# Kernel optimization log

Measured on AMD Instinct MI355X. Metric: run time of the kernel, lower is better.

The kernel has to match this reference:

```python
import jax, jax.numpy as jnp
import numpy as np
from functools import partial

H = 51

def lstm_cell(x, h, c, W_ih, W_hh, b_ih, b_hh):
    # PyTorch LSTMCell: gates ordered (i, f, g, o)
    z = x @ W_ih.T + b_ih + h @ W_hh.T + b_hh  # [B, 4H]
    i, f, g, o = jnp.split(z, 4, axis=-1)
    i = jax.nn.sigmoid(i)
    f = jax.nn.sigmoid(f)
    g = jnp.tanh(g)
    o = jax.nn.sigmoid(o)
    c_new = f * c + i * g
    h_new = o * jnp.tanh(c_new)
    return h_new, c_new


def setup_inputs() -> dict:
    key = jax.random.key(0)
    ks = jax.random.split(key, 12)
    B, T = 2048, 512
    s = 1.0 / np.sqrt(H)  # PyTorch default init scale
    inp = {
        "input": jax.random.normal(ks[0], (B, T), dtype=jnp.float32),
        "W_ih1": jax.random.uniform(ks[1], (4 * H, 1), jnp.float32, -s, s),
        "W_hh1": jax.random.uniform(ks[2], (4 * H, H), jnp.float32, -s, s),
        "b_ih1": jax.random.uniform(ks[3], (4 * H,), jnp.float32, -s, s),
        "b_hh1": jax.random.uniform(ks[4], (4 * H,), jnp.float32, -s, s),
        "W_ih2": jax.random.uniform(ks[5], (4 * H, H), jnp.float32, -s, s),
        "W_hh2": jax.random.uniform(ks[6], (4 * H, H), jnp.float32, -s, s),
        "b_ih2": jax.random.uniform(ks[7], (4 * H,), jnp.float32, -s, s),
        "b_hh2": jax.random.uniform(ks[8], (4 * H,), jnp.float32, -s, s),
        "W_lin": jax.random.uniform(ks[9], (1, H), jnp.float32, -s, s),
        "b_lin": jax.random.uniform(ks[10], (1,), jnp.float32, -s, s),
        "future": 32,
    }
    return inp


def reference(input, W_ih1, W_hh1, b_ih1, b_hh1, W_ih2, W_hh2, b_ih2, b_hh2, W_lin, b_lin, future):
    B, T = input.shape
    dt = input.dtype
    h1 = jnp.zeros((B, H), dt)
    c1 = jnp.zeros((B, H), dt)
    h2 = jnp.zeros((B, H), dt)
    c2 = jnp.zeros((B, H), dt)

    def core(carry, x_t):
        h1, c1, h2, c2 = carry
        h1, c1 = lstm_cell(x_t, h1, c1, W_ih1, W_hh1, b_ih1, b_hh1)
        h2, c2 = lstm_cell(h1, h2, c2, W_ih2, W_hh2, b_ih2, b_hh2)
        out = h2 @ W_lin.T + b_lin  # [B, 1]
        return (h1, c1, h2, c2), out

    xs = input.T[:, :, None]  # [T, B, 1]
    carry, outs = jax.lax.scan(core, (h1, c1, h2, c2), xs)

    def fstep(carry, _):
        state, out = carry
        new_state, new_out = core(state, out)
        return (new_state, new_out), new_out

    last_out = outs[-1]
    _, fouts = jax.lax.scan(fstep, (carry, last_out), None, length=future)

    all_outs = jnp.concatenate([outs, fouts], axis=0)  # [T+future, B, 1]
    return all_outs[:, :, 0].T  # [B, T+future]
```

## Files before the change

kernel.cpp:

```cpp
#include <hip/hip_runtime.h>

#define H 51
#define TIN 512
#define TTOT 544
#define BTILE 8
#define AST 88
#define H2ST 13
#define SOST 548
#define NTHR 768

typedef __attribute__((ext_vector_type(8))) short short8;
typedef __attribute__((ext_vector_type(4))) float float4v;

#define MFMA __builtin_amdgcn_mfma_f32_16x16x32_bf16

__device__ __forceinline__ float fast_rcp(float x) { return __builtin_amdgcn_rcpf(x); }
__device__ __forceinline__ float sigf(float x)  { return fast_rcp(1.0f + __expf(-x)); }
__device__ __forceinline__ float tanhf_(float x){ return 1.0f - 2.0f * fast_rcp(1.0f + __expf(2.0f * x)); }

__device__ __forceinline__ unsigned short bf16rnd(float x) {
    unsigned int u = __float_as_uint(x);
    return (unsigned short)((u + 0x7fffu + ((u >> 16) & 1u)) >> 16);
}
__device__ __forceinline__ unsigned int bf16pk(float a, float b) {
    unsigned int r;
    asm("v_cvt_pk_bf16_f32 %0, %1, %2" : "=v"(r) : "v"(a), "v"(b));
    return r;
}
__device__ __forceinline__ void bf16split(float x, unsigned short& hi, float& lo) {
    unsigned int u  = __float_as_uint(x);
    unsigned int hr = (u + 0x7fffu + ((u >> 16) & 1u)) & 0xffff0000u;
    hi = (unsigned short)(hr >> 16);
    lo = x - __uint_as_float(hr);
}

__device__ __forceinline__ float b1val(int k, int u, int g,
                                       const float* Whh1, const float* Wih1) {
    if (u >= H) return 0.0f;
    const int r = g * H + u;
    if (k < H)  return Whh1[r * H + k];
    if (k == H) return Wih1[r];
    return 0.0f;
}
__device__ __forceinline__ float b2val(int k, int u, int g,
                                       const float* Wih2, const float* Whh2) {
    if (u >= H) return 0.0f;
    const int r = g * H + u;
    if (k < H) return Wih2[r * H + k];
    if (k >= 64 && k < 64 + H) return Whh2[r * H + (k - 64)];
    return 0.0f;
}

__global__ __launch_bounds__(NTHR)
__attribute__((amdgpu_waves_per_eu(3, 3)))
void lstm_seq(
    const float* __restrict__ input,
    const float* __restrict__ W_ih1,
    const float* __restrict__ W_hh1,
    const float* __restrict__ b_ih1,
    const float* __restrict__ b_hh1,
    const float* __restrict__ W_ih2,
    const float* __restrict__ W_hh2,
    const float* __restrict__ b_ih2,
    const float* __restrict__ b_hh2,
    const float* __restrict__ W_lin,
    const float* __restrict__ b_lin,
    float* __restrict__ out)
{
    __shared__ __align__(16) unsigned short sA1h[2][16][AST];
    __shared__ __align__(16) unsigned short sA2h[2][16][AST];
    __shared__ float sH2f[2][64][H2ST];
    __shared__ __align__(8) float sXlo[2][8];
    __shared__ float sWlin[64];
    __shared__ __align__(16) float sIn[BTILE][TIN];
    __shared__ __align__(16) float sOut[BTILE][SOST];

    const int tid  = threadIdx.x;
    const int lane = tid & 63;
    const int wv   = tid >> 6;
    const int ut   = wv & 3;
    const int quad = lane >> 4;
    const int kq   = quad * 8;
    const int nl   = lane & 15;
    const int u    = ut * 16 + nl;
    const int ur   = (u < H) ? u : (H - 1);
    const int b0   = blockIdx.x * BTILE;
    const float blin = b_lin[0];
    const int rowA = (quad & 1) * 4 + (quad >> 1) * 2;
    const int arow = quad * 4;
    const int kc   = lane & 31;
    const int bhead= 2 * ut + (lane >> 5);

    {
        unsigned short* p0 = &sA1h[0][0][0];
        unsigned short* p2 = &sA2h[0][0][0];
        for (int i = tid; i < 2 * 16 * AST; i += NTHR) { p0[i] = 0; p2[i] = 0; }
        float* pf = &sH2f[0][0][0];
        for (int i = tid; i < 2 * 64 * H2ST; i += NTHR) pf[i] = 0.0f;
        if (tid < 16) sXlo[tid >> 3][tid & 7] = 0.0f;
        if (tid < 64) sWlin[tid] = (tid < H) ? W_lin[tid] : 0.0f;
        for (int i = tid; i < BTILE * (TIN / 4); i += NTHR) {
            const int r = i >> 7, c = i & 127;
            *(float4v*)&sIn[r][c * 4] =
                *(const float4v*)&input[(size_t)(b0 + r) * TIN + c * 4];
        }
    }
    __syncthreads();
    if (tid < 8) {
        unsigned short hh; float lo;
        bf16split(sIn[tid][0], hh, lo);
        sA1h[0][(tid & 2) ? tid + 6 : tid][51] = hh;
        sXlo[0][tid] = lo;
    }
    __syncthreads();

    if (wv < 4) {
        short8 B1h[4][2];
        float zb1[4], wxf[4];
        #pragma unroll
        for (int g = 0; g < 4; ++g) {
            #pragma unroll
            for (int kt = 0; kt < 2; ++kt)
                #pragma unroll
                for (int j = 0; j < 8; ++j)
                    B1h[g][kt][j] = (short)bf16rnd(b1val(kt * 32 + kq + j, u, g, W_hh1, W_ih1));
            const int r = g * H + ur;
            zb1[g] = b_ih1[r] + b_hh1[r];
            wxf[g] = W_ih1[r];
        }
        float c1[2] = {0, 0};

        auto l1work = [&](int rs, int ws) __attribute__((always_inline)) {
            short8 a0h = *(const short8*)&sA1h[rs][nl][kq];
            short8 a1h = *(const short8*)&sA1h[rs][nl][32 + kq];
            float2 xl = *(const float2*)&sXlo[rs][rowA];
            float4v C[4];
            #pragma unroll
            for (int g = 0; g < 4; ++g) {
                float4v c = {zb1[g], zb1[g], zb1[g], zb1[g]};
                c = MFMA(a0h, B1h[g][0], c, 0, 0, 0);
                c = MFMA(a1h, B1h[g][1], c, 0, 0, 0);
                C[g] = c;
            }
            float h1v[2];
            #pragma unroll
            for (int j = 0; j < 2; ++j) {
                const float xr = j ? xl.y : xl.x;
                float I = sigf  (C[0][j] + wxf[0] * xr);
                float F = sigf  (C[1][j] + wxf[1] * xr);
                float G = tanhf_(C[2][j] + wxf[2] * xr);
                float O = sigf  (C[3][j] + wxf[3] * xr);
                c1[j] = F * c1[j] + I * G;
                h1v[j] = O * tanhf_(c1[j]);
            }
            if (u < H) {
                const unsigned int pk = bf16pk(h1v[0], h1v[1]);
                sA1h[ws][arow][u]     = (unsigned short)pk;
                sA1h[ws][arow + 1][u] = (unsigned short)(pk >> 16);
            }
        };

        for (int s = 0; s < TIN; ++s) {
            if ((s & 1) == 0) l1work(0, 1);
            else              l1work(1, 0);
            __syncthreads();
        }
        for (int s = TIN; s <= TTOT; ++s) {
            const int rs = s & 1, ws = rs ^ 1;
            __syncthreads();
            __syncthreads();
            if (s < TTOT) l1work(rs, ws);
            __syncthreads();
        }
    } else if (wv < 8) {
        short8 B2h[4][4];
        float zb2[4];
        #pragma unroll
        for (int g = 0; g < 4; ++g) {
            #pragma unroll
            for (int kt = 0; kt < 4; ++kt)
                #pragma unroll
                for (int j = 0; j < 8; ++j)
                    B2h[g][kt][j] = (short)bf16rnd(b2val(kt * 32 + kq + j, u, g, W_ih2, W_hh2));
            const int r = g * H + ur;
            zb2[g] = b_ih2[r] + b_hh2[r];
        }
        float c2[2] = {0, 0};

        auto l2work = [&](int rs, int ws) __attribute__((always_inline)) {
            short8 f0h = *(const short8*)&sA1h[rs][nl][kq];
            short8 f1h = *(const short8*)&sA1h[rs][nl][32 + kq];
            short8 f2h = *(const short8*)&sA2h[rs][nl][kq];
            short8 f3h = *(const short8*)&sA2h[rs][nl][32 + kq];
            float4v C[4];
            #pragma unroll
            for (int g = 0; g < 4; ++g) {
                float4v c = {zb2[g], zb2[g], zb2[g], zb2[g]};
                c = MFMA(f0h, B2h[g][0], c, 0, 0, 0);
                c = MFMA(f1h, B2h[g][1], c, 0, 0, 0);
                c = MFMA(f2h, B2h[g][2], c, 0, 0, 0);
                c = MFMA(f3h, B2h[g][3], c, 0, 0, 0);
                C[g] = c;
            }
            float h2v[2];
            #pragma unroll
            for (int j = 0; j < 2; ++j) {
                float I = sigf  (C[0][j]);
                float F = sigf  (C[1][j]);
                float G = tanhf_(C[2][j]);
                float O = sigf  (C[3][j]);
                c2[j] = F * c2[j] + I * G;
                h2v[j] = O * tanhf_(c2[j]);
            }
            if (u < H) {
                const unsigned int pk = bf16pk(h2v[0], h2v[1]);
                sA2h[ws][arow][u]     = (unsigned short)pk;
                sA2h[ws][arow + 1][u] = (unsigned short)(pk >> 16);
                sH2f[rs][u][rowA]     = h2v[0];
                sH2f[rs][u][rowA + 1] = h2v[1];
            }
        };

        for (int s = 0; s < TIN; ++s) {
            if ((s & 1) == 0) { if (s) l2work(0, 1); }
            else              l2work(1, 0);
            __syncthreads();
        }
        for (int s = TIN; s <= TTOT; ++s) {
            const int rs = s & 1, ws = rs ^ 1;
            l2work(rs, ws);
            __syncthreads();
            __syncthreads();
            __syncthreads();
        }
    } else {
        auto headw = [&](int slot, int outt) __attribute__((always_inline)) -> float {
            float p = sWlin[kc]      * sH2f[slot][kc][bhead]
                    + sWlin[kc + 32] * sH2f[slot][kc + 32][bhead];
            p += __shfl_xor(p, 1);  p += __shfl_xor(p, 2);  p += __shfl_xor(p, 4);
            p += __shfl_xor(p, 8);  p += __shfl_xor(p, 16);
            float val = p + blin;
            if (kc == 0) sOut[bhead][outt] = val;
            return val;
        };

        for (int s = 0; s < TIN; ++s) {
            const int ws = (s & 1) ? 0 : 1;
            if (s >= 2) headw(ws, s - 2);
            if ((wv == 8) && (lane < 8) && (s + 1 < TIN)) {
                unsigned short hh; float lo; bf16split(sIn[lane][s + 1], hh, lo);
                sA1h[ws][(lane & 2) ? lane + 6 : lane][51] = hh;
                sXlo[ws][lane] = lo;
            }
            __syncthreads();
        }
        for (int s = TIN; s <= TTOT; ++s) {
            const int rs = s & 1, ws = rs ^ 1;
            __syncthreads();
            {
                float val = headw(rs, s - 1);
                if (kc == 0 && s < TTOT) {
                    unsigned short hh; float lo; bf16split(val, hh, lo);
                    sA1h[rs][(bhead & 2) ? bhead + 6 : bhead][51] = hh;
                    sXlo[rs][bhead] = lo;
                }
                if (s == TIN) headw(ws, s - 2);
            }
            __syncthreads();
            __syncthreads();
        }
    }

    __syncthreads();
    for (int i = tid; i < BTILE * (TTOT / 4); i += NTHR) {
        const int r = i / (TTOT / 4);
        const int c = i - r * (TTOT / 4);
        *(float4v*)&out[(size_t)(b0 + r) * TTOT + c * 4] =
            *(const float4v*)&sOut[r][c * 4];
    }
}

extern "C" void kernel_launch(void* const* d_in, const int* in_sizes, int n_in,
                              void* d_out, int out_size, void* d_ws, size_t ws_size,
                              hipStream_t stream) {
    const float* input = (const float*)d_in[0];
    const float* W_ih1 = (const float*)d_in[1];
    const float* W_hh1 = (const float*)d_in[2];
    const float* b_ih1 = (const float*)d_in[3];
    const float* b_hh1 = (const float*)d_in[4];
    const float* W_ih2 = (const float*)d_in[5];
    const float* W_hh2 = (const float*)d_in[6];
    const float* b_ih2 = (const float*)d_in[7];
    const float* b_hh2 = (const float*)d_in[8];
    const float* W_lin = (const float*)d_in[9];
    const float* b_lin = (const float*)d_in[10];
    float* out = (float*)d_out;

    lstm_seq<<<dim3(256), dim3(NTHR), 0, stream>>>(input, W_ih1, W_hh1, b_ih1, b_hh1,
                                                   W_ih2, W_hh2, b_ih2, b_hh2,
                                                   W_lin, b_lin, out);
}
```

Before: 390.3 us.

## Replace block barriers with LDS counter spin-waits and triple buffering in teacher-forced phase

In the 512-step input phase, the per-step __syncthreads between the layer-1, layer-2 and head warp groups are replaced by shared-memory counters. Each group bumps its counter after a step and spin-waits (with s_sleep) on the counters it depends on. The state buffers go from double to triple slots, so producers can run one step ahead of consumers without overwriting data still being read. This aims to decouple the groups and hide barrier stalls, at the cost of polling overhead and subtle memory-ordering risk, since it relies on lgkmcnt waits and volatile reads.

After: 469.8 us. +20.4%, slower.

```diff
diff --git a/kernel.cpp b/kernel.cpp
--- a/kernel.cpp
+++ b/kernel.cpp
@@ -8,6 +8,7 @@
 #define H2ST 13
 #define SOST 548
 #define NTHR 768
+#define NSLOT 3
 
 typedef __attribute__((ext_vector_type(8))) short short8;
 typedef __attribute__((ext_vector_type(4))) float float4v;
@@ -67,13 +68,14 @@
     const float* __restrict__ b_lin,
     float* __restrict__ out)
 {
-    __shared__ __align__(16) unsigned short sA1h[2][16][AST];
-    __shared__ __align__(16) unsigned short sA2h[2][16][AST];
-    __shared__ float sH2f[2][64][H2ST];
-    __shared__ __align__(8) float sXlo[2][8];
+    __shared__ __align__(16) unsigned short sA1h[NSLOT][16][AST];
+    __shared__ __align__(16) unsigned short sA2h[NSLOT][16][AST];
+    __shared__ float sH2f[NSLOT][64][H2ST];
+    __shared__ __align__(8) float sXlo[NSLOT][8];
     __shared__ float sWlin[64];
     __shared__ __align__(16) float sIn[BTILE][TIN];
     __shared__ __align__(16) float sOut[BTILE][SOST];
+    __shared__ int sCnt[4];
 
     const int tid  = threadIdx.x;
     const int lane = tid & 63;
@@ -91,14 +93,25 @@
     const int kc   = lane & 31;
     const int bhead= 2 * ut + (lane >> 5);
 
+    volatile int* vc = (volatile int*)sCnt;
+    auto spin = [&](int idx, int v) __attribute__((always_inline)) {
+        while (vc[idx] < v) __builtin_amdgcn_s_sleep(1);
+        asm volatile("" ::: "memory");
+    };
+    auto bump = [&](int idx) __attribute__((always_inline)) {
+        asm volatile("s_waitcnt lgkmcnt(0)" ::: "memory");
+        if (lane == 0) atomicAdd(&sCnt[idx], 1);
+    };
+
     {
         unsigned short* p0 = &sA1h[0][0][0];
         unsigned short* p2 = &sA2h[0][0][0];
-        for (int i = tid; i < 2 * 16 * AST; i += NTHR) { p0[i] = 0; p2[i] = 0; }
+        for (int i = tid; i < NSLOT * 16 * AST; i += NTHR) { p0[i] = 0; p2[i] = 0; }
         float* pf = &sH2f[0][0][0];
-        for (int i = tid; i < 2 * 64 * H2ST; i += NTHR) pf[i] = 0.0f;
-        if (tid < 16) sXlo[tid >> 3][tid & 7] = 0.0f;
+        for (int i = tid; i < NSLOT * 64 * H2ST; i += NTHR) pf[i] = 0.0f;
+        if (tid < NSLOT * 8) sXlo[tid >> 3][tid & 7] = 0.0f;
         if (tid < 64) sWlin[tid] = (tid < H) ? W_lin[tid] : 0.0f;
+        if (tid == 0) { sCnt[0] = 0; sCnt[1] = 4; sCnt[2] = 0; }
         for (int i = tid; i < BTILE * (TIN / 4); i += NTHR) {
             const int r = i >> 7, c = i & 127;
             *(float4v*)&sIn[r][c * 4] =
@@ -160,13 +173,19 @@
             }
         };
 
-        for (int s = 0; s < TIN; ++s) {
-            if ((s & 1) == 0) l1work(0, 1);
-            else              l1work(1, 0);
-            __syncthreads();
-        }
+        {
+            int si = 0, so = 1, t1 = 0;
+            for (int s = 0; s < TIN; ++s) {
+                spin(0, t1); spin(2, t1); spin(1, t1 - 4);
+                l1work(si, so);
+                bump(0);
+                t1 += 4;
+                si = so; so = (so == 2) ? 0 : so + 1;
+            }
+        }
+        __syncthreads();
         for (int s = TIN; s <= TTOT; ++s) {
-            const int rs = s & 1, ws = rs ^ 1;
+            const int rs = s % 3, ws = (s + 1) % 3;
             __syncthreads();
             __syncthreads();
             if (s < TTOT) l1work(rs, ws);
@@ -221,13 +240,19 @@
             }
         };
 
-        for (int s = 0; s < TIN; ++s) {
-            if ((s & 1) == 0) { if (s) l2work(0, 1); }
-            else              l2work(1, 0);
-            __syncthreads();
-        }
+        {
+            int si = 1, so = 2, t4 = 4;
+            for (int t = 1; t < TIN; ++t) {
+                spin(0, t4); spin(1, t4); spin(2, t4 - 4);
+                l2work(si, so);
+                bump(1);
+                t4 += 4;
+                si = so; so = (so == 2) ? 0 : so + 1;
+            }
+        }
+        __syncthreads();
         for (int s = TIN; s <= TTOT; ++s) {
-            const int rs = s & 1, ws = rs ^ 1;
+            const int rs = s % 3, ws = (s + 1) % 3;
             l2work(rs, ws);
             __syncthreads();
             __syncthreads();
@@ -244,18 +269,25 @@
             return val;
         };
 
-        for (int s = 0; s < TIN; ++s) {
-            const int ws = (s & 1) ? 0 : 1;
-            if (s >= 2) headw(ws, s - 2);
-            if ((wv == 8) && (lane < 8) && (s + 1 < TIN)) {
-                unsigned short hh; float lo; bf16split(sIn[lane][s + 1], hh, lo);
-                sA1h[ws][(lane & 2) ? lane + 6 : lane][51] = hh;
-                sXlo[ws][lane] = lo;
-            }
-            __syncthreads();
-        }
+        {
+            int sm1 = 2, so = 1, t4 = 0;
+            for (int s = 0; s < TIN; ++s) {
+                spin(0, t4 - 4);
+                if (s >= 2) { spin(1, t4); headw(sm1, s - 2); }
+                if ((wv == 8) && (lane < 8) && (s + 1 < TIN)) {
+                    unsigned short hh; float lo; bf16split(sIn[lane][s + 1], hh, lo);
+                    sA1h[so][(lane & 2) ? lane + 6 : lane][51] = hh;
+                    sXlo[so][lane] = lo;
+                }
+                bump(2);
+                t4 += 4;
+                sm1 = (sm1 == 2) ? 0 : sm1 + 1;
+                so  = (so  == 2) ? 0 : so + 1;
+            }
+        }
+        __syncthreads();
         for (int s = TIN; s <= TTOT; ++s) {
-            const int rs = s & 1, ws = rs ^ 1;
+            const int rs = s % 3;
             __syncthreads();
             {
                 float val = headw(rs, s - 1);
@@ -264,7 +296,7 @@
                     sA1h[rs][(bhead & 2) ? bhead + 6 : bhead][51] = hh;
                     sXlo[rs][bhead] = lo;
                 }
-                if (s == TIN) headw(ws, s - 2);
+                if (s == TIN) headw((TIN - 1) % 3, s - 2);
             }
             __syncthreads();
             __syncthreads();
```

## Split LSTM gate nonlinearities across duplicated wave groups and merge head into layer-1 waves

Applied to the files above, without the earlier changes.

Raises the block to 16 waves: each layer now runs on two 4-wave groups that issue the same MFMAs, and each group handles only one of the two accumulator rows, which halves the per-thread transcendental work on the critical path. The separate head/input-feed waves are removed. The second layer-1 group now also computes the linear head and stages the next input. This trades redundant MFMA work and more waves per block for a shorter serial elementwise tail per timestep. The sIn row is padded so the input load becomes a single pass per thread.

Result: slower. 535.8 us (+37.3%).

```diff
diff --git a/kernel.cpp b/kernel.cpp
--- a/kernel.cpp
+++ b/kernel.cpp
@@ -6,8 +6,9 @@
 #define BTILE 8
 #define AST 88
 #define H2ST 13
+#define INST 516
 #define SOST 548
-#define NTHR 768
+#define NTHR 1024
 
 typedef __attribute__((ext_vector_type(8))) short short8;
 typedef __attribute__((ext_vector_type(4))) float float4v;
@@ -21,11 +22,6 @@
 __device__ __forceinline__ unsigned short bf16rnd(float x) {
     unsigned int u = __float_as_uint(x);
     return (unsigned short)((u + 0x7fffu + ((u >> 16) & 1u)) >> 16);
-}
-__device__ __forceinline__ unsigned int bf16pk(float a, float b) {
-    unsigned int r;
-    asm("v_cvt_pk_bf16_f32 %0, %1, %2" : "=v"(r) : "v"(a), "v"(b));
-    return r;
 }
 __device__ __forceinline__ void bf16split(float x, unsigned short& hi, float& lo) {
     unsigned int u  = __float_as_uint(x);
@@ -52,7 +48,7 @@
 }
 
 __global__ __launch_bounds__(NTHR)
-__attribute__((amdgpu_waves_per_eu(3, 3)))
+__attribute__((amdgpu_waves_per_eu(4, 4)))
 void lstm_seq(
     const float* __restrict__ input,
     const float* __restrict__ W_ih1,
@@ -72,13 +68,15 @@
     __shared__ float sH2f[2][64][H2ST];
     __shared__ __align__(8) float sXlo[2][8];
     __shared__ float sWlin[64];
-    __shared__ __align__(16) float sIn[BTILE][TIN];
+    __shared__ __align__(16) float sIn[BTILE][INST];
     __shared__ __align__(16) float sOut[BTILE][SOST];
 
     const int tid  = threadIdx.x;
     const int lane = tid & 63;
     const int wv   = tid >> 6;
+    const int grp  = wv >> 2;
     const int ut   = wv & 3;
+    const int jj   = grp & 1;
     const int quad = lane >> 4;
     const int kq   = quad * 8;
     const int nl   = lane & 15;
@@ -86,8 +84,8 @@
     const int ur   = (u < H) ? u : (H - 1);
     const int b0   = blockIdx.x * BTILE;
     const float blin = b_lin[0];
-    const int rowA = (quad & 1) * 4 + (quad >> 1) * 2;
-    const int arow = quad * 4;
+    const int rowAj = (quad & 1) * 4 + (quad >> 1) * 2 + jj;
+    const int arowj = quad * 4 + jj;
     const int kc   = lane & 31;
     const int bhead= 2 * ut + (lane >> 5);
 
@@ -99,8 +97,8 @@
         for (int i = tid; i < 2 * 64 * H2ST; i += NTHR) pf[i] = 0.0f;
         if (tid < 16) sXlo[tid >> 3][tid & 7] = 0.0f;
         if (tid < 64) sWlin[tid] = (tid < H) ? W_lin[tid] : 0.0f;
-        for (int i = tid; i < BTILE * (TIN / 4); i += NTHR) {
-            const int r = i >> 7, c = i & 127;
+        {
+            const int r = tid >> 7, c = tid & 127;
             *(float4v*)&sIn[r][c * 4] =
                 *(const float4v*)&input[(size_t)(b0 + r) * TIN + c * 4];
         }
@@ -114,7 +112,7 @@
     }
     __syncthreads();
 
-    if (wv < 4) {
+    if (grp < 2) {
         short8 B1h[4][2];
         float zb1[4], wxf[4];
         #pragma unroll
@@ -128,12 +126,12 @@
             zb1[g] = b_ih1[r] + b_hh1[r];
             wxf[g] = W_ih1[r];
         }
-        float c1[2] = {0, 0};
+        float c1 = 0.0f;
 
         auto l1work = [&](int rs, int ws) __attribute__((always_inline)) {
             short8 a0h = *(const short8*)&sA1h[rs][nl][kq];
             short8 a1h = *(const short8*)&sA1h[rs][nl][32 + kq];
-            float2 xl = *(const float2*)&sXlo[rs][rowA];
+            float xr = sXlo[rs][rowAj];
             float4v C[4];
             #pragma unroll
             for (int g = 0; g < 4; ++g) {
@@ -142,98 +140,14 @@
                 c = MFMA(a1h, B1h[g][1], c, 0, 0, 0);
                 C[g] = c;
             }
-            float h1v[2];
-            #pragma unroll
-            for (int j = 0; j < 2; ++j) {
-                const float xr = j ? xl.y : xl.x;
-                float I = sigf  (C[0][j] + wxf[0] * xr);
-                float F = sigf  (C[1][j] + wxf[1] * xr);
-                float G = tanhf_(C[2][j] + wxf[2] * xr);
-                float O = sigf  (C[3][j] + wxf[3] * xr);
-                c1[j] = F * c1[j] + I * G;
-                h1v[j] = O * tanhf_(c1[j]);
-            }
-            if (u < H) {
-                const unsigned int pk = bf16pk(h1v[0], h1v[1]);
-                sA1h[ws][arow][u]     = (unsigned short)pk;
-                sA1h[ws][arow + 1][u] = (unsigned short)(pk >> 16);
-            }
+            float I = sigf  (C[0][jj] + wxf[0] * xr);
+            float F = sigf  (C[1][jj] + wxf[1] * xr);
+            float G = tanhf_(C[2][jj] + wxf[2] * xr);
+            float O = sigf  (C[3][jj] + wxf[3] * xr);
+            c1 = F * c1 + I * G;
+            float h1v = O * tanhf_(c1);
+            if (u < H) sA1h[ws][arowj][u] = bf16rnd(h1v);
         };
-
-        for (int s = 0; s < TIN; ++s) {
-            if ((s & 1) == 0) l1work(0, 1);
-            else              l1work(1, 0);
-            __syncthreads();
-        }
-        for (int s = TIN; s <= TTOT; ++s) {
-            const int rs = s & 1, ws = rs ^ 1;
-            __syncthreads();
-            __syncthreads();
-            if (s < TTOT) l1work(rs, ws);
-            __syncthreads();
-        }
-    } else if (wv < 8) {
-        short8 B2h[4][4];
-        float zb2[4];
-        #pragma unroll
-        for (int g = 0; g < 4; ++g) {
-            #pragma unroll
-            for (int kt = 0; kt < 4; ++kt)
-                #pragma unroll
-                for (int j = 0; j < 8; ++j)
-                    B2h[g][kt][j] = (short)bf16rnd(b2val(kt * 32 + kq + j, u, g, W_ih2, W_hh2));
-            const int r = g * H + ur;
-            zb2[g] = b_ih2[r] + b_hh2[r];
-        }
-        float c2[2] = {0, 0};
-
-        auto l2work = [&](int rs, int ws) __attribute__((always_inline)) {
-            short8 f0h = *(const short8*)&sA1h[rs][nl][kq];
-            short8 f1h = *(const short8*)&sA1h[rs][nl][32 + kq];
-            short8 f2h = *(const short8*)&sA2h[rs][nl][kq];
-            short8 f3h = *(const short8*)&sA2h[rs][nl][32 + kq];
-            float4v C[4];
-            #pragma unroll
-            for (int g = 0; g < 4; ++g) {
-                float4v c = {zb2[g], zb2[g], zb2[g], zb2[g]};
-                c = MFMA(f0h, B2h[g][0], c, 0, 0, 0);
-                c = MFMA(f1h, B2h[g][1], c, 0, 0, 0);
-                c = MFMA(f2h, B2h[g][2], c, 0, 0, 0);
-                c = MFMA(f3h, B2h[g][3], c, 0, 0, 0);
-                C[g] = c;
-            }
-            float h2v[2];
-            #pragma unroll
-            for (int j = 0; j < 2; ++j) {
-                float I = sigf  (C[0][j]);
-                float F = sigf  (C[1][j]);
-                float G = tanhf_(C[2][j]);
-                float O = sigf  (C[3][j]);
-                c2[j] = F * c2[j] + I * G;
-                h2v[j] = O * tanhf_(c2[j]);
-            }
-            if (u < H) {
-                const unsigned int pk = bf16pk(h2v[0], h2v[1]);
-                sA2h[ws][arow][u]     = (unsigned short)pk;
-                sA2h[ws][arow + 1][u] = (unsigned short)(pk >> 16);
-                sH2f[rs][u][rowA]     = h2v[0];
-                sH2f[rs][u][rowA + 1] = h2v[1];
-            }
-        };
-
-        for (int s = 0; s < TIN; ++s) {
-            if ((s & 1) == 0) { if (s) l2work(0, 1); }
-            else              l2work(1, 0);
-            __syncthreads();
-        }
-        for (int s = TIN; s <= TTOT; ++s) {
-            const int rs = s & 1, ws = rs ^ 1;
-            l2work(rs, ws);
-            __syncthreads();
-            __syncthreads();
-            __syncthreads();
-        }
-    } else {
         auto headw = [&](int slot, int outt) __attribute__((always_inline)) -> float {
             float p = sWlin[kc]      * sH2f[slot][kc][bhead]
                     + sWlin[kc + 32] * sH2f[slot][kc + 32][bhead];
@@ -244,20 +158,32 @@
             return val;
         };
 
-        for (int s = 0; s < TIN; ++s) {
-            const int ws = (s & 1) ? 0 : 1;
-            if (s >= 2) headw(ws, s - 2);
-            if ((wv == 8) && (lane < 8) && (s + 1 < TIN)) {
-                unsigned short hh; float lo; bf16split(sIn[lane][s + 1], hh, lo);
-                sA1h[ws][(lane & 2) ? lane + 6 : lane][51] = hh;
-                sXlo[ws][lane] = lo;
-            }
-            __syncthreads();
+        if (grp == 0) {
+            for (int s = 0; s < TIN; ++s) {
+                if ((s & 1) == 0) l1work(0, 1);
+                else              l1work(1, 0);
+                __syncthreads();
+            }
+        } else {
+            for (int s = 0; s < TIN; ++s) {
+                const int rs = s & 1, ws = rs ^ 1;
+                float xpre = 0.0f;
+                const bool doX = (wv == 4) && (lane < 8) && (s + 1 < TIN);
+                if (doX) xpre = sIn[lane][s + 1];
+                if (s >= 2) headw(ws, s - 2);
+                l1work(rs, ws);
+                if (doX) {
+                    unsigned short hh; float lo; bf16split(xpre, hh, lo);
+                    sA1h[ws][(lane & 2) ? lane + 6 : lane][51] = hh;
+                    sXlo[ws][lane] = lo;
+                }
+                __syncthreads();
+            }
         }
         for (int s = TIN; s <= TTOT; ++s) {
             const int rs = s & 1, ws = rs ^ 1;
             __syncthreads();
-            {
+            if (grp == 1) {
                 float val = headw(rs, s - 1);
                 if (kc == 0 && s < TTOT) {
                     unsigned short hh; float lo; bf16split(val, hh, lo);
@@ -266,6 +192,61 @@
                 }
                 if (s == TIN) headw(ws, s - 2);
             }
+            __syncthreads();
+            if (s < TTOT) l1work(rs, ws);
+            __syncthreads();
+        }
+    } else {
+        short8 B2h[4][4];
+        float zb2[4];
+        #pragma unroll
+        for (int g = 0; g < 4; ++g) {
+            #pragma unroll
+            for (int kt = 0; kt < 4; ++kt)
+                #pragma unroll
+                for (int j = 0; j < 8; ++j)
+                    B2h[g][kt][j] = (short)bf16rnd(b2val(kt * 32 + kq + j, u, g, W_ih2, W_hh2));
+            const int r = g * H + ur;
+            zb2[g] = b_ih2[r] + b_hh2[r];
+        }
+        float c2 = 0.0f;
+
+        auto l2work = [&](int rs, int ws) __attribute__((always_inline)) {
+            short8 f0h = *(const short8*)&sA1h[rs][nl][kq];
+            short8 f1h = *(const short8*)&sA1h[rs][nl][32 + kq];
+            short8 f2h = *(const short8*)&sA2h[rs][nl][kq];
+            short8 f3h = *(const short8*)&sA2h[rs][nl][32 + kq];
+            float4v C[4];
+            #pragma unroll
+            for (int g = 0; g < 4; ++g) {
+                float4v c = {zb2[g], zb2[g], zb2[g], zb2[g]};
+                c = MFMA(f0h, B2h[g][0], c, 0, 0, 0);
+                c = MFMA(f1h, B2h[g][1], c, 0, 0, 0);
+                c = MFMA(f2h, B2h[g][2], c, 0, 0, 0);
+                c = MFMA(f3h, B2h[g][3], c, 0, 0, 0);
+                C[g] = c;
+            }
+            float I = sigf  (C[0][jj]);
+            float F = sigf  (C[1][jj]);
+            float G = tanhf_(C[2][jj]);
+            float O = sigf  (C[3][jj]);
+            c2 = F * c2 + I * G;
+            float h2v = O * tanhf_(c2);
+            if (u < H) {
+                sA2h[ws][arowj][u] = bf16rnd(h2v);
+                sH2f[rs][u][rowAj] = h2v;
+            }
+        };
+
+        for (int s = 0; s < TIN; ++s) {
+            if ((s & 1) == 0) { if (s) l2work(0, 1); }
+            else              l2work(1, 0);
+            __syncthreads();
+        }
+        for (int s = TIN; s <= TTOT; ++s) {
+            const int rs = s & 1, ws = rs ^ 1;
+            l2work(rs, ws);
+            __syncthreads();
             __syncthreads();
             __syncthreads();
         }
```

## Replace per-step block barriers with group-local LDS counters and 4-slot buffers

Applied to the files above, without the earlier changes.

In the teacher-forced phase, layer-1 and layer-2 wave groups now synchronise within each group through LDS atomic counters with spin-waits, and hit a full block barrier only every two timesteps. The h1, h2-float and x buffers are widened from 2 to 4 slots so producers can run ahead without overwriting data still in use. The goal is to cut the cost of the per-step __syncthreads across 12 waves on the serial recurrence. The cost is spin-wait polling with s_sleep, more LDS, and a more fragile slot-indexing scheme that could hide races.

New measurement: 407.4 us. +4.4%, slower.

```diff
diff --git a/kernel.cpp b/kernel.cpp
--- a/kernel.cpp
+++ b/kernel.cpp
@@ -5,7 +5,8 @@
 #define TTOT 544
 #define BTILE 8
 #define AST 88
-#define H2ST 13
+#define H2ST 9
+#define INST 516
 #define SOST 548
 #define NTHR 768
 
@@ -67,17 +68,19 @@
     const float* __restrict__ b_lin,
     float* __restrict__ out)
 {
-    __shared__ __align__(16) unsigned short sA1h[2][16][AST];
+    __shared__ __align__(16) unsigned short sA1h[4][16][AST];
     __shared__ __align__(16) unsigned short sA2h[2][16][AST];
-    __shared__ float sH2f[2][64][H2ST];
-    __shared__ __align__(8) float sXlo[2][8];
+    __shared__ float sH2f[4][64][H2ST];
+    __shared__ __align__(8) float sXlo[4][8];
     __shared__ float sWlin[64];
-    __shared__ __align__(16) float sIn[BTILE][TIN];
+    __shared__ __align__(16) float sIn[BTILE][INST];
     __shared__ __align__(16) float sOut[BTILE][SOST];
+    __shared__ int sCnt[2];
 
     const int tid  = threadIdx.x;
     const int lane = tid & 63;
     const int wv   = tid >> 6;
+    const int grp  = wv >> 2;
     const int ut   = wv & 3;
     const int quad = lane >> 4;
     const int kq   = quad * 8;
@@ -91,14 +94,28 @@
     const int kc   = lane & 31;
     const int bhead= 2 * ut + (lane >> 5);
 
+    volatile int* vc = (volatile int*)sCnt;
+    auto gwait = [&](int idx, int v) __attribute__((always_inline)) {
+        if (lane == 0) {
+            while (vc[idx] < v) __builtin_amdgcn_s_sleep(1);
+        }
+        asm volatile("" ::: "memory");
+    };
+    auto gbump = [&](int idx) __attribute__((always_inline)) {
+        asm volatile("s_waitcnt lgkmcnt(0)" ::: "memory");
+        if (lane == 0) atomicAdd(&sCnt[idx], 1);
+    };
+
     {
         unsigned short* p0 = &sA1h[0][0][0];
+        for (int i = tid; i < 4 * 16 * AST; i += NTHR) p0[i] = 0;
         unsigned short* p2 = &sA2h[0][0][0];
-        for (int i = tid; i < 2 * 16 * AST; i += NTHR) { p0[i] = 0; p2[i] = 0; }
+        for (int i = tid; i < 2 * 16 * AST; i += NTHR) p2[i] = 0;
         float* pf = &sH2f[0][0][0];
-        for (int i = tid; i < 2 * 64 * H2ST; i += NTHR) pf[i] = 0.0f;
-        if (tid < 16) sXlo[tid >> 3][tid & 7] = 0.0f;
+        for (int i = tid; i < 4 * 64 * H2ST; i += NTHR) pf[i] = 0.0f;
+        if (tid < 32) sXlo[tid >> 3][tid & 7] = 0.0f;
         if (tid < 64) sWlin[tid] = (tid < H) ? W_lin[tid] : 0.0f;
+        if (tid < 2) sCnt[tid] = 0;
         for (int i = tid; i < BTILE * (TIN / 4); i += NTHR) {
             const int r = i >> 7, c = i & 127;
             *(float4v*)&sIn[r][c * 4] =
@@ -106,15 +123,16 @@
         }
     }
     __syncthreads();
-    if (tid < 8) {
+    if (tid < 16) {
+        const int st = tid >> 3, b = tid & 7;
         unsigned short hh; float lo;
-        bf16split(sIn[tid][0], hh, lo);
-        sA1h[0][(tid & 2) ? tid + 6 : tid][51] = hh;
-        sXlo[0][tid] = lo;
+        bf16split(sIn[b][st], hh, lo);
+        sA1h[(st - 1) & 3][(b & 2) ? b + 6 : b][51] = hh;
+        sXlo[(st - 1) & 3][b] = lo;
     }
     __syncthreads();
 
-    if (wv < 4) {
+    if (grp == 0) {
         short8 B1h[4][2];
         float zb1[4], wxf[4];
         #pragma unroll
@@ -160,19 +178,25 @@
             }
         };
 
-        for (int s = 0; s < TIN; ++s) {
-            if ((s & 1) == 0) l1work(0, 1);
-            else              l1work(1, 0);
-            __syncthreads();
-        }
-        for (int s = TIN; s <= TTOT; ++s) {
-            const int rs = s & 1, ws = rs ^ 1;
-            __syncthreads();
-            __syncthreads();
-            if (s < TTOT) l1work(rs, ws);
-            __syncthreads();
-        }
-    } else if (wv < 8) {
+        for (int w = 0; w < TIN / 2; ++w) {
+            const int s0 = 2 * w;
+            gwait(0, 4 * s0);
+            l1work((s0 - 1) & 3, s0 & 3);
+            gbump(0);
+            gwait(0, 4 * (s0 + 1));
+            l1work(s0 & 3, (s0 + 1) & 3);
+            gbump(0);
+            __syncthreads();
+        }
+        __syncthreads();
+        __syncthreads();
+        for (int s = TIN; s < TTOT; ++s) {
+            l1work((s - 1) & 3, s & 3);
+            __syncthreads();
+            __syncthreads();
+            __syncthreads();
+        }
+    } else if (grp == 1) {
         short8 B2h[4][4];
         float zb2[4];
         #pragma unroll
@@ -187,11 +211,11 @@
         }
         float c2[2] = {0, 0};
 
-        auto l2work = [&](int rs, int ws) __attribute__((always_inline)) {
-            short8 f0h = *(const short8*)&sA1h[rs][nl][kq];
-            short8 f1h = *(const short8*)&sA1h[rs][nl][32 + kq];
-            short8 f2h = *(const short8*)&sA2h[rs][nl][kq];
-            short8 f3h = *(const short8*)&sA2h[rs][nl][32 + kq];
+        auto l2work = [&](int ra, int rh, int wh, int wf) __attribute__((always_inline)) {
+            short8 f0h = *(const short8*)&sA1h[ra][nl][kq];
+            short8 f1h = *(const short8*)&sA1h[ra][nl][32 + kq];
+            short8 f2h = *(const short8*)&sA2h[rh][nl][kq];
+            short8 f3h = *(const short8*)&sA2h[rh][nl][32 + kq];
             float4v C[4];
             #pragma unroll
             for (int g = 0; g < 4; ++g) {
@@ -214,22 +238,29 @@
             }
             if (u < H) {
                 const unsigned int pk = bf16pk(h2v[0], h2v[1]);
-                sA2h[ws][arow][u]     = (unsigned short)pk;
-                sA2h[ws][arow + 1][u] = (unsigned short)(pk >> 16);
-                sH2f[rs][u][rowA]     = h2v[0];
-                sH2f[rs][u][rowA + 1] = h2v[1];
+                sA2h[wh][arow][u]     = (unsigned short)pk;
+                sA2h[wh][arow + 1][u] = (unsigned short)(pk >> 16);
+                sH2f[wf][u][rowA]     = h2v[0];
+                sH2f[wf][u][rowA + 1] = h2v[1];
             }
         };
-
-        for (int s = 0; s < TIN; ++s) {
-            if ((s & 1) == 0) { if (s) l2work(0, 1); }
-            else              l2work(1, 0);
-            __syncthreads();
-        }
-        for (int s = TIN; s <= TTOT; ++s) {
-            const int rs = s & 1, ws = rs ^ 1;
-            l2work(rs, ws);
-            __syncthreads();
+        auto l2step = [&](int s) __attribute__((always_inline)) {
+            gwait(1, 4 * s);
+            l2work(s & 3, (s - 1) & 1, s & 1, s & 3);
+            gbump(1);
+        };
+
+        for (int w = 0; w < TIN / 2; ++w) {
+            if (w >= 1) { l2step(2 * w - 2); l2step(2 * w - 1); }
+            __syncthreads();
+        }
+        l2step(TIN - 2);
+        l2step(TIN - 1);
+        __syncthreads();
+        __syncthreads();
+        for (int s = TIN; s < TTOT; ++s) {
+            __syncthreads();
+            l2work(s & 3, (s - 1) & 1, s & 1, s & 3);
             __syncthreads();
             __syncthreads();
         }
@@ -244,29 +275,45 @@
             return val;
         };
 
-        for (int s = 0; s < TIN; ++s) {
-            const int ws = (s & 1) ? 0 : 1;
-            if (s >= 2) headw(ws, s - 2);
-            if ((wv == 8) && (lane < 8) && (s + 1 < TIN)) {
-                unsigned short hh; float lo; bf16split(sIn[lane][s + 1], hh, lo);
-                sA1h[ws][(lane & 2) ? lane + 6 : lane][51] = hh;
-                sXlo[ws][lane] = lo;
-            }
-            __syncthreads();
-        }
-        for (int s = TIN; s <= TTOT; ++s) {
-            const int rs = s & 1, ws = rs ^ 1;
-            __syncthreads();
-            {
-                float val = headw(rs, s - 1);
-                if (kc == 0 && s < TTOT) {
-                    unsigned short hh; float lo; bf16split(val, hh, lo);
-                    sA1h[rs][(bhead & 2) ? bhead + 6 : bhead][51] = hh;
-                    sXlo[rs][bhead] = lo;
+        for (int w = 0; w < TIN / 2; ++w) {
+            if (w >= 2) {
+                headw((2 * w - 4) & 3, 2 * w - 4);
+                headw((2 * w - 3) & 3, 2 * w - 3);
+            }
+            if (wv == 8 && lane < 16) {
+                const int ts = 2 * w + 2 + (lane >> 3);
+                const int b  = lane & 7;
+                if (ts < TIN) {
+                    unsigned short hh; float lo;
+                    bf16split(sIn[b][ts], hh, lo);
+                    sA1h[(ts - 1) & 3][(b & 2) ? b + 6 : b][51] = hh;
+                    sXlo[(ts - 1) & 3][b] = lo;
                 }
-                if (s == TIN) headw(ws, s - 2);
-            }
-            __syncthreads();
+            }
+            __syncthreads();
+        }
+        headw((TIN - 4) & 3, TIN - 4);
+        headw((TIN - 3) & 3, TIN - 3);
+        __syncthreads();
+        headw((TIN - 2) & 3, TIN - 2);
+        {
+            float val = headw((TIN - 1) & 3, TIN - 1);
+            if (kc == 0) {
+                unsigned short hh; float lo; bf16split(val, hh, lo);
+                sA1h[(TIN - 1) & 3][(bhead & 2) ? bhead + 6 : bhead][51] = hh;
+                sXlo[(TIN - 1) & 3][bhead] = lo;
+            }
+        }
+        __syncthreads();
+        for (int s = TIN; s < TTOT; ++s) {
+            __syncthreads();
+            __syncthreads();
+            float val = headw(s & 3, s);
+            if (kc == 0 && s + 1 < TTOT) {
+                unsigned short hh; float lo; bf16split(val, hh, lo);
+                sA1h[s & 3][(bhead & 2) ? bhead + 6 : bhead][51] = hh;
+                sXlo[s & 3][bhead] = lo;
+            }
             __syncthreads();
         }
     }
```
